# Kernel tuning notes

Hardware: AMD Instinct MI355X
Metric: run time of the kernel (lower is better)

## Reference

```python
import jax, jax.numpy as jnp
import numpy as np

N = 50000      # nodes
E = 800000     # edges (avg degree 16)
F_IN = 128     # num_node_features
D = 64         # embedding_size (= per-head out_channels)
H = 4          # heads
ED = 20        # edge_dim (hardcoded in module)
SLOPE = 0.2    # GATv2 leaky_relu negative slope
N_LAYERS = 3   # conv applied 3 times with shared weights


def setup_inputs() -> dict:
    key = jax.random.key(0)
    ks = jax.random.split(key, 12)
    s = 0.1
    return {
        "x": jax.random.normal(ks[0], (N, F_IN), jnp.float32),
        "edge_attr": jax.random.normal(ks[1], (E, 2), jnp.float32),
        "edge_index": jax.random.randint(ks[2], (2, E), 0, N, dtype=jnp.int32),
        # f: Linear(F_IN, D)
        "f_W": jax.random.normal(ks[3], (F_IN, D), jnp.float32) * s,
        "f_b": jnp.zeros((D,), jnp.float32),
        # fe: Linear(2, ED)
        "fe_W": jax.random.normal(ks[4], (2, ED), jnp.float32) * s,
        "fe_b": jnp.zeros((ED,), jnp.float32),
        # GATv2Conv lin_l / lin_r: Linear(D, H*D)
        "Wl": jax.random.normal(ks[5], (D, H * D), jnp.float32) * s,
        "bl": jnp.zeros((H * D,), jnp.float32),
        "Wr": jax.random.normal(ks[6], (D, H * D), jnp.float32) * s,
        "br": jnp.zeros((H * D,), jnp.float32),
        # lin_edge: Linear(ED, H*D, bias=False)
        "We": jax.random.normal(ks[7], (ED, H * D), jnp.float32) * s,
        # attention vector att: [H, D]
        "att": jax.random.normal(ks[8], (H, D), jnp.float32) * s,
        # final bias (concat=False -> size D)
        "bias": jnp.zeros((D,), jnp.float32),
    }


def _gatv2_conv(h, e_emb, src, dst, Wl, bl, Wr, br, We, att, bias):
    # h: [N, D], e_emb: [E, ED], src/dst: [E]
    xl = (h @ Wl + bl).reshape(-1, H, D)        # source transform  [N,H,D]
    xr = (h @ Wr + br).reshape(-1, H, D)        # target transform  [N,H,D]
    ee = (e_emb @ We).reshape(-1, H, D)         # edge transform    [E,H,D]
    m = jax.nn.leaky_relu(xl[src] + xr[dst] + ee, SLOPE)  # [E,H,D]
    score = jnp.einsum('ehd,hd->eh', m, att)    # [E,H]
    # segment softmax over incoming edges of each dst node
    smax = jax.ops.segment_max(score, dst, num_segments=N)   # [N,H]
    ex = jnp.exp(score - smax[dst])
    denom = jax.ops.segment_sum(ex, dst, num_segments=N)     # [N,H]
    alpha = ex / denom[dst]                                  # [E,H]
    out = jax.ops.segment_sum(alpha[:, :, None] * xl[src], dst, num_segments=N)  # [N,H,D]
    return out.mean(axis=1) + bias              # concat=False -> head mean, [N,D]


def reference(x, edge_attr, edge_index, f_W, f_b, fe_W, fe_b, Wl, bl, Wr, br, We, att, bias):
    src, dst = edge_index[0], edge_index[1]
    h = jax.nn.relu(x @ f_W + f_b)
    e = jax.nn.relu(edge_attr @ fe_W + fe_b)
    for _ in range(N_LAYERS):
        h = jax.nn.relu(_gatv2_conv(h, e, src, dst, Wl, bl, Wr, br, We, att, bias))
    return h
```

## Files before the change

### kernel.cpp

```cpp
#include <hip/hip_runtime.h>
#include <math.h>

typedef float v2f __attribute__((ext_vector_type(2)));

#define LN2_INV 1.4426950408889634f

__device__ __forceinline__ float fexp2(float x) {
#if __has_builtin(__builtin_amdgcn_exp2f)
    return __builtin_amdgcn_exp2f(x);
#else
    return exp2f(x);
#endif
}

__device__ __forceinline__ int rdlane_i(int v, int k) {
    return __builtin_amdgcn_readlane(v, k);
}

__device__ __forceinline__ v2f max2(v2f a, float b) {
    v2f r; r.x = fmaxf(a.x, b); r.y = fmaxf(a.y, b); return r;
}
__device__ __forceinline__ v2f min2(v2f a, float b) {
    v2f r; r.x = fminf(a.x, b); r.y = fminf(a.y, b); return r;
}

#define DPP_ROW_ADD(V, CTRL) \
    V += __int_as_float(__builtin_amdgcn_update_dpp(0, __float_as_int(V), CTRL, 0xf, 0xf, true));

__global__ __launch_bounds__(256) void k_h0(const float* __restrict__ x,
                                            const float* __restrict__ fW,
                                            const float* __restrict__ fb,
                                            float* __restrict__ h0) {
    __shared__ __align__(16) float xs[8 * 128];
    int t = threadIdx.x;
    int base = blockIdx.x * 8;
#pragma unroll
    for (int r = 0; r < 4; ++r) { int j = r * 256 + t; xs[j] = x[base * 128 + j]; }
    __syncthreads();
    int c = t & 63, half = t >> 6;
    float acc0 = fb[c], acc1 = fb[c];
    int m0 = half, m1 = half + 4;
#pragma unroll 8
    for (int k0 = 0; k0 < 128; k0 += 4) {
        float4 a = *(const float4*)&xs[m0 * 128 + k0];
        float4 b = *(const float4*)&xs[m1 * 128 + k0];
        float w0 = fW[(k0 + 0) * 64 + c], w1 = fW[(k0 + 1) * 64 + c];
        float w2 = fW[(k0 + 2) * 64 + c], w3 = fW[(k0 + 3) * 64 + c];
        acc0 = fmaf(a.x, w0, fmaf(a.y, w1, fmaf(a.z, w2, fmaf(a.w, w3, acc0))));
        acc1 = fmaf(b.x, w0, fmaf(b.y, w1, fmaf(b.z, w2, fmaf(b.w, w3, acc1))));
    }
    h0[(base + m0) * 64 + c] = fmaxf(acc0, 0.f);
    h0[(base + m1) * 64 + c] = fmaxf(acc1, 0.f);
}

__global__ __launch_bounds__(256) void k_xlxr(const float* __restrict__ h,
                                              const float* __restrict__ Wl,
                                              const float* __restrict__ Wr,
                                              const float* __restrict__ bl,
                                              const float* __restrict__ br,
                                              float* __restrict__ xl,
                                              float* __restrict__ xr) {
    __shared__ __align__(16) float hs[16 * 64];
    int t = threadIdx.x;
    int base = blockIdx.x * 16;
#pragma unroll
    for (int r = 0; r < 4; ++r) hs[r * 256 + t] = h[base * 64 + r * 256 + t];
    __syncthreads();
    float bL = bl[t], bR = br[t];
    float accl[16], accr[16];
#pragma unroll
    for (int m = 0; m < 16; ++m) { accl[m] = bL; accr[m] = bR; }
#pragma unroll 4
    for (int k0 = 0; k0 < 64; k0 += 4) {
        float wl[4], wr[4];
#pragma unroll
        for (int q = 0; q < 4; ++q) {
            wl[q] = Wl[(k0 + q) * 256 + t];
            wr[q] = Wr[(k0 + q) * 256 + t];
        }
#pragma unroll
        for (int m = 0; m < 16; ++m) {
            float4 hv = *(const float4*)&hs[m * 64 + k0];
            accl[m] = fmaf(hv.x, wl[0], fmaf(hv.y, wl[1], fmaf(hv.z, wl[2], fmaf(hv.w, wl[3], accl[m]))));
            accr[m] = fmaf(hv.x, wr[0], fmaf(hv.y, wr[1], fmaf(hv.z, wr[2], fmaf(hv.w, wr[3], accr[m]))));
        }
    }
#pragma unroll
    for (int m = 0; m < 16; ++m) {
        xl[(base + m) * 256 + t] = accl[m];
        xr[(base + m) * 256 + t] = accr[m];
    }
}

__global__ void k_zero(int* __restrict__ deg, int* __restrict__ counter, int Nn) {
    int i = blockIdx.x * 256 + threadIdx.x;
    if (i < Nn) deg[i] = 0;
    if (i == 0) *counter = 0;
}

__global__ void k_count(const int* __restrict__ dstArr, int* __restrict__ deg, int Ee) {
    int e = blockIdx.x * 256 + threadIdx.x;
    if (e < Ee) atomicAdd(&deg[dstArr[e]], 1);
}

__global__ void k_alloc(const int* __restrict__ deg, int* __restrict__ counter,
                        int* __restrict__ start, int* __restrict__ cursor, int Nn) {
    int n = blockIdx.x * 256 + threadIdx.x;
    if (n < Nn) {
        int d = deg[n];
        int b = atomicAdd(counter, d);
        start[n] = b;
        cursor[n] = b;
    }
}

__global__ void k_fill(const int* __restrict__ dstArr, const int* __restrict__ srcArr,
                       const float* __restrict__ eattr, const float* __restrict__ feW,
                       const float* __restrict__ feb, int* __restrict__ cursor,
                       int* __restrict__ rec, int Ee) {
    int e = blockIdx.x * 256 + threadIdx.x;
    if (e >= Ee) return;
    float a0 = eattr[2 * e], a1 = eattr[2 * e + 1];
    int p = atomicAdd(&cursor[dstArr[e]], 1);
    float* r = (float*)(rec + (size_t)p * 24);
    float s[20];
#pragma unroll
    for (int k = 0; k < 20; ++k)
        s[k] = fmaxf(fmaf(a0, feW[k], fmaf(a1, feW[20 + k], feb[k])), 0.f);
#pragma unroll
    for (int j = 0; j < 5; ++j)
        ((float4*)r)[j] = make_float4(s[4 * j], s[4 * j + 1], s[4 * j + 2], s[4 * j + 3]);
    ((int*)r)[20] = srcArr[e];
}

__global__ __launch_bounds__(256, 3) void k_edge(
    const float4* __restrict__ xl4p, const float4* __restrict__ xr4p,
    const float* __restrict__ att, const float4* __restrict__ We4,
    const int* __restrict__ rec, const int* __restrict__ start,
    const int* __restrict__ deg, const float* __restrict__ bias,
    float* __restrict__ hout, int Nn) {
    const int lane = threadIdx.x & 63;
    const int n = (int)((blockIdx.x * 256u + threadIdx.x) >> 6);
    if (n >= Nn) return;

    const int dn = __builtin_amdgcn_readfirstlane(deg[n]);
    float4 bias4 = ((const float4*)bias)[lane & 15];
    if (dn == 0) {
        if (lane < 16) {
            float4 o = make_float4(fmaxf(bias4.x, 0.f), fmaxf(bias4.y, 0.f),
                                   fmaxf(bias4.z, 0.f), fmaxf(bias4.w, 0.f));
            ((float4*)hout)[(size_t)n * 16 + lane] = o;
        }
        return;
    }
    const int s0 = __builtin_amdgcn_readfirstlane(start[n]);
    const int* rb = rec + (size_t)s0 * 24 + (lane & 31);

    float4 attv = ((const float4*)att)[lane];
    v2f att01 = {attv.x * LN2_INV, attv.y * LN2_INV};
    v2f att23 = {attv.z * LN2_INV, attv.w * LN2_INV};
    v2f at201 = 0.2f * att01, at223 = 0.2f * att23;
    float4 xrv = xr4p[(size_t)n * 64 + lane];
    v2f xr01 = {xrv.x, xrv.y}, xr23 = {xrv.z, xrv.w};
    v2f we01[20], we23[20];
#pragma unroll
    for (int k = 0; k < 20; ++k) {
        float4 w = We4[k * 64 + lane];
        we01[k].x = w.x; we01[k].y = w.y;
        we23[k].x = w.z; we23[k].y = w.w;
    }
    const int bperm = ((lane & 48) | 15) << 2;

    v2f acc01 = {0.f, 0.f}, acc23 = {0.f, 0.f};
    float l = 0.f;

    int i1 = dn > 1 ? 1 : 0;
    int rv0 = rb[0];
    int rv1 = rb[(size_t)i1 * 24];
    int src0 = rdlane_i(rv0, 20);
    float4 xl0 = xl4p[(size_t)src0 * 64 + lane];

    for (int i = 0; i < dn; ++i) {
        int i2 = (i + 2 < dn) ? (i + 2) : (dn - 1);
        int rv2 = rb[(size_t)i2 * 24];
        int src1 = rdlane_i(rv1, 20);
        float4 xl1 = xl4p[(size_t)src1 * 64 + lane];

        v2f xl01 = {xl0.x, xl0.y}, xl23 = {xl0.z, xl0.w};

        v2f ee01, ee23;
        {
            float sk = __int_as_float(rdlane_i(rv0, 0));
            ee01 = sk * we01[0];
            ee23 = sk * we23[0];
        }
#pragma unroll
        for (int k = 1; k < 20; ++k) {
            float sk = __int_as_float(rdlane_i(rv0, k));
            ee01 += sk * we01[k];
            ee23 += sk * we23[k];
        }

        v2f v01 = (xl01 + xr01) + ee01;
        v2f v23 = (xl23 + xr23) + ee23;
        v2f p01 = att01 * max2(v01, 0.f) + at201 * min2(v01, 0.f);
        v2f p23 = att23 * max2(v23, 0.f) + at223 * min2(v23, 0.f);
        v2f pr = p01 + p23;
        float ps = pr.x + pr.y;
        DPP_ROW_ADD(ps, 0x111)
        DPP_ROW_ADD(ps, 0x112)
        DPP_ROW_ADD(ps, 0x114)
        DPP_ROW_ADD(ps, 0x118)
        float sc = __int_as_float(
            __builtin_amdgcn_ds_bpermute(bperm, __float_as_int(ps)));
        float w_ = fexp2(sc);
        l += w_;
        acc01 += w_ * xl01;
        acc23 += w_ * xl23;

        rv0 = rv1; rv1 = rv2; xl0 = xl1;
    }

    float inv = 0.25f / l;
    float4 r = make_float4(acc01.x * inv, acc01.y * inv, acc23.x * inv, acc23.y * inv);
    r.x += __shfl_xor(r.x, 16, 64); r.x += __shfl_xor(r.x, 32, 64);
    r.y += __shfl_xor(r.y, 16, 64); r.y += __shfl_xor(r.y, 32, 64);
    r.z += __shfl_xor(r.z, 16, 64); r.z += __shfl_xor(r.z, 32, 64);
    r.w += __shfl_xor(r.w, 16, 64); r.w += __shfl_xor(r.w, 32, 64);
    if (lane < 16) {
        float4 o = make_float4(fmaxf(r.x + bias4.x, 0.f), fmaxf(r.y + bias4.y, 0.f),
                               fmaxf(r.z + bias4.z, 0.f), fmaxf(r.w + bias4.w, 0.f));
        ((float4*)hout)[(size_t)n * 16 + lane] = o;
    }
}

extern "C" void kernel_launch(void* const* d_in, const int* in_sizes, int n_in,
                              void* d_out, int out_size, void* d_ws, size_t ws_size,
                              hipStream_t stream) {
    const float* x     = (const float*)d_in[0];
    const float* eattr = (const float*)d_in[1];
    const int*   eidx  = (const int*)d_in[2];
    const float* fW    = (const float*)d_in[3];
    const float* fb    = (const float*)d_in[4];
    const float* feW   = (const float*)d_in[5];
    const float* feb   = (const float*)d_in[6];
    const float* Wl    = (const float*)d_in[7];
    const float* bl    = (const float*)d_in[8];
    const float* Wr    = (const float*)d_in[9];
    const float* br    = (const float*)d_in[10];
    const float* We    = (const float*)d_in[11];
    const float* att   = (const float*)d_in[12];
    const float* bias  = (const float*)d_in[13];
    float* out = (float*)d_out;

    const int N = in_sizes[0] / 128;
    const int E = in_sizes[1] / 2;
    const int* srcArr = eidx;
    const int* dstArr = eidx + E;

    char* p = (char*)d_ws;
    auto alloc = [&](size_t bytes) -> char* {
        char* r = p;
        p += (bytes + 255) & ~(size_t)255;
        return r;
    };
    float* hA   = (float*)alloc((size_t)N * 64 * 4);
    float* hB   = (float*)alloc((size_t)N * 64 * 4);
    float* xl   = (float*)alloc((size_t)N * 256 * 4);
    float* xr   = (float*)alloc((size_t)N * 256 * 4);
    int* deg    = (int*)alloc((size_t)N * 4);
    int* start  = (int*)alloc((size_t)N * 4);
    int* cursor = (int*)alloc((size_t)N * 4);
    int* counter = (int*)alloc(256);
    int* rec    = (int*)alloc((size_t)E * 24 * 4);

    k_h0<<<N / 8, 256, 0, stream>>>(x, fW, fb, hA);
    k_zero<<<(N + 255) / 256, 256, 0, stream>>>(deg, counter, N);
    k_count<<<(E + 255) / 256, 256, 0, stream>>>(dstArr, deg, E);
    k_alloc<<<(N + 255) / 256, 256, 0, stream>>>(deg, counter, start, cursor, N);
    k_fill<<<(E + 255) / 256, 256, 0, stream>>>(dstArr, srcArr, eattr, feW, feb,
                                                cursor, rec, E);

    const float* hin = hA;
    for (int layer = 0; layer < 3; ++layer) {
        float* hout = (layer == 2) ? out : ((layer == 0) ? hB : hA);
        k_xlxr<<<N / 16, 256, 0, stream>>>(hin, Wl, Wr, bl, br, xl, xr);
        k_edge<<<(N * 64) / 256, 256, 0, stream>>>(
            (const float4*)xl, (const float4*)xr, att, (const float4*)We,
            rec, start, deg, bias, hout, N);
        hin = hout;
    }
}
```

Before: 919.2 us.

## Process edges in groups of four with LDS-staged edge weights

The edge kernel now stages the edge-transform weights We in LDS per block instead of holding them in 40 registers per lane. It handles incoming edges four at a time, software-pipelining the record loads and source-row gathers of the next group behind the current group's math. Partial tail groups are masked by zeroing their softmax weight. Leaky-relu is rewritten as a*v + b*|v| with attention and log2 scaling folded in. The aim is to amortise weight reads across four edges, expose more memory-level parallelism and cut register pressure, at the cost of extra LDS reads, redundant work on masked tail edges, and a block-wide barrier before the early return.

```diff
diff --git a/kernel.cpp b/kernel.cpp
--- a/kernel.cpp
+++ b/kernel.cpp
@@ -15,13 +15,6 @@
 
 __device__ __forceinline__ int rdlane_i(int v, int k) {
     return __builtin_amdgcn_readlane(v, k);
-}
-
-__device__ __forceinline__ v2f max2(v2f a, float b) {
-    v2f r; r.x = fmaxf(a.x, b); r.y = fmaxf(a.y, b); return r;
-}
-__device__ __forceinline__ v2f min2(v2f a, float b) {
-    v2f r; r.x = fminf(a.x, b); r.y = fminf(a.y, b); return r;
 }
 
 #define DPP_ROW_ADD(V, CTRL) \
@@ -139,8 +132,14 @@
     const int* __restrict__ rec, const int* __restrict__ start,
     const int* __restrict__ deg, const float* __restrict__ bias,
     float* __restrict__ hout, int Nn) {
-    const int lane = threadIdx.x & 63;
-    const int n = (int)((blockIdx.x * 256u + threadIdx.x) >> 6);
+    __shared__ __align__(16) float4 swe[20 * 64];
+    const int t = threadIdx.x;
+#pragma unroll
+    for (int j = 0; j < 5; ++j) swe[j * 256 + t] = We4[j * 256 + t];
+    __syncthreads();
+
+    const int lane = t & 63;
+    const int n = (int)((blockIdx.x * 256u + t) >> 6);
     if (n >= Nn) return;
 
     const int dn = __builtin_amdgcn_readfirstlane(deg[n]);
@@ -157,69 +156,126 @@
     const int* rb = rec + (size_t)s0 * 24 + (lane & 31);
 
     float4 attv = ((const float4*)att)[lane];
-    v2f att01 = {attv.x * LN2_INV, attv.y * LN2_INV};
-    v2f att23 = {attv.z * LN2_INV, attv.w * LN2_INV};
-    v2f at201 = 0.2f * att01, at223 = 0.2f * att23;
+    float4 aA = make_float4(0.6f * LN2_INV * attv.x, 0.6f * LN2_INV * attv.y,
+                            0.6f * LN2_INV * attv.z, 0.6f * LN2_INV * attv.w);
+    float4 aB = make_float4(0.4f * LN2_INV * attv.x, 0.4f * LN2_INV * attv.y,
+                            0.4f * LN2_INV * attv.z, 0.4f * LN2_INV * attv.w);
     float4 xrv = xr4p[(size_t)n * 64 + lane];
     v2f xr01 = {xrv.x, xrv.y}, xr23 = {xrv.z, xrv.w};
-    v2f we01[20], we23[20];
-#pragma unroll
-    for (int k = 0; k < 20; ++k) {
-        float4 w = We4[k * 64 + lane];
-        we01[k].x = w.x; we01[k].y = w.y;
-        we23[k].x = w.z; we23[k].y = w.w;
-    }
     const int bperm = ((lane & 48) | 15) << 2;
 
     v2f acc01 = {0.f, 0.f}, acc23 = {0.f, 0.f};
     float l = 0.f;
 
-    int i1 = dn > 1 ? 1 : 0;
-    int rv0 = rb[0];
-    int rv1 = rb[(size_t)i1 * 24];
-    int src0 = rdlane_i(rv0, 20);
-    float4 xl0 = xl4p[(size_t)src0 * 64 + lane];
-
-    for (int i = 0; i < dn; ++i) {
-        int i2 = (i + 2 < dn) ? (i + 2) : (dn - 1);
-        int rv2 = rb[(size_t)i2 * 24];
-        int src1 = rdlane_i(rv1, 20);
-        float4 xl1 = xl4p[(size_t)src1 * 64 + lane];
-
-        v2f xl01 = {xl0.x, xl0.y}, xl23 = {xl0.z, xl0.w};
-
-        v2f ee01, ee23;
+    const int nfull = dn >> 2;
+    const int rem = dn & 3;
+    const int ngroups = nfull + (rem ? 1 : 0);
+    const int fb = dn >= 4 ? dn - 4 : 0;
+
+#define LOAD_GROUP(RV, B)                                                   \
+    {                                                                       \
+        _Pragma("unroll")                                                   \
+        for (int j_ = 0; j_ < 4; ++j_) {                                    \
+            int idx_ = (B) + j_;                                            \
+            idx_ = idx_ < dn ? idx_ : dn - 1;                               \
+            RV[j_] = rb[(size_t)idx_ * 24];                                 \
+        }                                                                   \
+    }
+#define GATHER_GROUP(XL, RV)                                                \
+    {                                                                       \
+        _Pragma("unroll")                                                   \
+        for (int j_ = 0; j_ < 4; ++j_) {                                    \
+            int src_ = rdlane_i(RV[j_], 20);                                \
+            XL[j_] = xl4p[(size_t)src_ * 64 + lane];                        \
+        }                                                                   \
+    }
+
+    int rvA[4], rvB[4];
+    float4 xlA[4], xlB[4];
+    int b0 = (nfull > 0) ? 0 : fb;
+    LOAD_GROUP(rvA, b0)
+    GATHER_GROUP(xlA, rvA)
+
+    for (int g = 0; g < ngroups; ++g) {
+        int gn = g + 1;
+        bool havenext = gn < ngroups;
+        if (havenext) {
+            int bn = (gn < nfull) ? (gn << 2) : fb;
+            LOAD_GROUP(rvB, bn)
+        }
+
+        v2f ee01[4], ee23[4];
         {
-            float sk = __int_as_float(rdlane_i(rv0, 0));
-            ee01 = sk * we01[0];
-            ee23 = sk * we23[0];
+            float4 w = swe[lane];
+            v2f w01 = {w.x, w.y}, w23 = {w.z, w.w};
+#pragma unroll
+            for (int j = 0; j < 4; ++j) {
+                float sk = __int_as_float(rdlane_i(rvA[j], 0));
+                ee01[j] = sk * w01;
+                ee23[j] = sk * w23;
+            }
         }
 #pragma unroll
         for (int k = 1; k < 20; ++k) {
-            float sk = __int_as_float(rdlane_i(rv0, k));
-            ee01 += sk * we01[k];
-            ee23 += sk * we23[k];
-        }
-
-        v2f v01 = (xl01 + xr01) + ee01;
-        v2f v23 = (xl23 + xr23) + ee23;
-        v2f p01 = att01 * max2(v01, 0.f) + at201 * min2(v01, 0.f);
-        v2f p23 = att23 * max2(v23, 0.f) + at223 * min2(v23, 0.f);
-        v2f pr = p01 + p23;
-        float ps = pr.x + pr.y;
-        DPP_ROW_ADD(ps, 0x111)
-        DPP_ROW_ADD(ps, 0x112)
-        DPP_ROW_ADD(ps, 0x114)
-        DPP_ROW_ADD(ps, 0x118)
-        float sc = __int_as_float(
-            __builtin_amdgcn_ds_bpermute(bperm, __float_as_int(ps)));
-        float w_ = fexp2(sc);
-        l += w_;
-        acc01 += w_ * xl01;
-        acc23 += w_ * xl23;
-
-        rv0 = rv1; rv1 = rv2; xl0 = xl1;
-    }
+            float4 w = swe[k * 64 + lane];
+            v2f w01 = {w.x, w.y}, w23 = {w.z, w.w};
+#pragma unroll
+            for (int j = 0; j < 4; ++j) {
+                float sk = __int_as_float(rdlane_i(rvA[j], k));
+                ee01[j] += sk * w01;
+                ee23[j] += sk * w23;
+            }
+        }
+
+        if (havenext) GATHER_GROUP(xlB, rvB)
+
+        int b = (g < nfull) ? (g << 2) : fb;
+        int lo = (g < nfull) ? b : (nfull << 2);
+        float ps[4];
+#pragma unroll
+        for (int j = 0; j < 4; ++j) {
+            v2f v01 = {xlA[j].x, xlA[j].y};
+            v2f v23 = {xlA[j].z, xlA[j].w};
+            v01 = (v01 + xr01) + ee01[j];
+            v23 = (v23 + xr23) + ee23[j];
+            float tt = aB.x * __builtin_fabsf(v01.x);
+            tt = fmaf(aA.x, v01.x, tt);
+            tt = fmaf(aB.y, __builtin_fabsf(v01.y), tt);
+            tt = fmaf(aA.y, v01.y, tt);
+            tt = fmaf(aB.z, __builtin_fabsf(v23.x), tt);
+            tt = fmaf(aA.z, v23.x, tt);
+            tt = fmaf(aB.w, __builtin_fabsf(v23.y), tt);
+            tt = fmaf(aA.w, v23.y, tt);
+            ps[j] = tt;
+        }
+#pragma unroll
+        for (int j = 0; j < 4; ++j) { DPP_ROW_ADD(ps[j], 0x111) }
+#pragma unroll
+        for (int j = 0; j < 4; ++j) { DPP_ROW_ADD(ps[j], 0x112) }
+#pragma unroll
+        for (int j = 0; j < 4; ++j) { DPP_ROW_ADD(ps[j], 0x114) }
+#pragma unroll
+        for (int j = 0; j < 4; ++j) { DPP_ROW_ADD(ps[j], 0x118) }
+#pragma unroll
+        for (int j = 0; j < 4; ++j) {
+            float sc = __int_as_float(
+                __builtin_amdgcn_ds_bpermute(bperm, __float_as_int(ps[j])));
+            float mk = (b + j >= lo && b + j < dn) ? 1.f : 0.f;
+            float w_ = fexp2(sc) * mk;
+            l += w_;
+            v2f xl01 = {xlA[j].x, xlA[j].y};
+            v2f xl23 = {xlA[j].z, xlA[j].w};
+            acc01 += w_ * xl01;
+            acc23 += w_ * xl23;
+        }
+
+        if (havenext) {
+#pragma unroll
+            for (int j = 0; j < 4; ++j) { rvA[j] = rvB[j]; xlA[j] = xlB[j]; }
+        }
+    }
+#undef LOAD_GROUP
+#undef GATHER_GROUP
 
     float inv = 0.25f / l;
     float4 r = make_float4(acc01.x * inv, acc01.y * inv, acc23.x * inv, acc23.y * inv);
@@ -272,7 +328,7 @@
     int* start  = (int*)alloc((size_t)N * 4);
     int* cursor = (int*)alloc((size_t)N * 4);
     int* counter = (int*)alloc(256);
-    int* rec    = (int*)alloc((size_t)E * 24 * 4);
+    int* rec    = (int*)alloc((size_t)E * 24 * 4 + 256);
 
     k_h0<<<N / 8, 256, 0, stream>>>(x, fW, fb, hA);
     k_zero<<<(N + 255) / 256, 256, 0, stream>>>(deg, counter, N);
```

Result: slower. 1.089 ms (+18.5%).

## Stage edge weights in LDS, process edges in pairs, simplify leaky-relu scoring

Applied to the files above, without the earlier changes.

Moves the 20x256 edge-transform weight matrix out of per-thread registers into shared memory loaded once per block, which frees registers so occupancy can rise to 4 blocks per SIMD. Edge records are now read as uniform scalar loads instead of per-lane loads plus readlane, and edges are processed two at a time with a two-edge prefetch of source features. The leaky-relu plus attention dot is rewritten as 0.6*att*v + 0.4*att*|v|, which saves min/max operations. In exchange every block pays an LDS fill and barrier, and each inner iteration adds LDS reads for the weights.

```diff
diff --git a/kernel.cpp b/kernel.cpp
--- a/kernel.cpp
+++ b/kernel.cpp
@@ -11,17 +11,6 @@
 #else
     return exp2f(x);
 #endif
-}
-
-__device__ __forceinline__ int rdlane_i(int v, int k) {
-    return __builtin_amdgcn_readlane(v, k);
-}
-
-__device__ __forceinline__ v2f max2(v2f a, float b) {
-    v2f r; r.x = fmaxf(a.x, b); r.y = fmaxf(a.y, b); return r;
-}
-__device__ __forceinline__ v2f min2(v2f a, float b) {
-    v2f r; r.x = fminf(a.x, b); r.y = fminf(a.y, b); return r;
 }
 
 #define DPP_ROW_ADD(V, CTRL) \
@@ -133,14 +122,20 @@
     ((int*)r)[20] = srcArr[e];
 }
 
-__global__ __launch_bounds__(256, 3) void k_edge(
+__global__ __launch_bounds__(256, 4) void k_edge(
     const float4* __restrict__ xl4p, const float4* __restrict__ xr4p,
     const float* __restrict__ att, const float4* __restrict__ We4,
     const int* __restrict__ rec, const int* __restrict__ start,
     const int* __restrict__ deg, const float* __restrict__ bias,
     float* __restrict__ hout, int Nn) {
-    const int lane = threadIdx.x & 63;
-    const int n = (int)((blockIdx.x * 256u + threadIdx.x) >> 6);
+    __shared__ __align__(16) float4 swe[20 * 64];
+    const int t = threadIdx.x;
+#pragma unroll
+    for (int j = 0; j < 5; ++j) swe[j * 256 + t] = We4[j * 256 + t];
+    __syncthreads();
+
+    const int lane = t & 63;
+    const int n = (int)((blockIdx.x * 256u + t) >> 6);
     if (n >= Nn) return;
 
     const int dn = __builtin_amdgcn_readfirstlane(deg[n]);
@@ -154,71 +149,109 @@
         return;
     }
     const int s0 = __builtin_amdgcn_readfirstlane(start[n]);
-    const int* rb = rec + (size_t)s0 * 24 + (lane & 31);
+    const float* __restrict__ rbf = (const float*)rec + (size_t)s0 * 24;
 
     float4 attv = ((const float4*)att)[lane];
-    v2f att01 = {attv.x * LN2_INV, attv.y * LN2_INV};
-    v2f att23 = {attv.z * LN2_INV, attv.w * LN2_INV};
-    v2f at201 = 0.2f * att01, at223 = 0.2f * att23;
+    float4 aA = make_float4(0.6f * LN2_INV * attv.x, 0.6f * LN2_INV * attv.y,
+                            0.6f * LN2_INV * attv.z, 0.6f * LN2_INV * attv.w);
+    float4 aB = make_float4(0.4f * LN2_INV * attv.x, 0.4f * LN2_INV * attv.y,
+                            0.4f * LN2_INV * attv.z, 0.4f * LN2_INV * attv.w);
     float4 xrv = xr4p[(size_t)n * 64 + lane];
     v2f xr01 = {xrv.x, xrv.y}, xr23 = {xrv.z, xrv.w};
-    v2f we01[20], we23[20];
-#pragma unroll
-    for (int k = 0; k < 20; ++k) {
-        float4 w = We4[k * 64 + lane];
-        we01[k].x = w.x; we01[k].y = w.y;
-        we23[k].x = w.z; we23[k].y = w.w;
-    }
     const int bperm = ((lane & 48) | 15) << 2;
 
     v2f acc01 = {0.f, 0.f}, acc23 = {0.f, 0.f};
     float l = 0.f;
 
-    int i1 = dn > 1 ? 1 : 0;
-    int rv0 = rb[0];
-    int rv1 = rb[(size_t)i1 * 24];
-    int src0 = rdlane_i(rv0, 20);
+    const int ngroups = (dn + 1) >> 1;
+
+    const float* r0 = rbf;
+    const float* r1 = rbf + (dn > 1 ? 24 : 0);
+    int src0 = ((const int*)r0)[20];
+    int src1 = ((const int*)r1)[20];
     float4 xl0 = xl4p[(size_t)src0 * 64 + lane];
-
-    for (int i = 0; i < dn; ++i) {
-        int i2 = (i + 2 < dn) ? (i + 2) : (dn - 1);
-        int rv2 = rb[(size_t)i2 * 24];
-        int src1 = rdlane_i(rv1, 20);
-        float4 xl1 = xl4p[(size_t)src1 * 64 + lane];
-
-        v2f xl01 = {xl0.x, xl0.y}, xl23 = {xl0.z, xl0.w};
-
-        v2f ee01, ee23;
+    float4 xl1 = xl4p[(size_t)src1 * 64 + lane];
+
+    for (int g = 0; g < ngroups; ++g) {
+        const bool havenext = (g + 1) < ngroups;
+        const float *nr0, *nr1;
+        float4 nxl0, nxl1;
+        if (havenext) {
+            int e0n = (g + 1) << 1;
+            int e1n = e0n + 1 < dn ? e0n + 1 : dn - 1;
+            nr0 = rbf + (size_t)e0n * 24;
+            nr1 = rbf + (size_t)e1n * 24;
+            int ns0 = ((const int*)nr0)[20];
+            int ns1 = ((const int*)nr1)[20];
+            nxl0 = xl4p[(size_t)ns0 * 64 + lane];
+            nxl1 = xl4p[(size_t)ns1 * 64 + lane];
+        }
+
+        v2f eA01, eA23, eB01, eB23;
         {
-            float sk = __int_as_float(rdlane_i(rv0, 0));
-            ee01 = sk * we01[0];
-            ee23 = sk * we23[0];
+            float4 w = swe[lane];
+            v2f w01 = {w.x, w.y}, w23 = {w.z, w.w};
+            float sa = r0[0], sb = r1[0];
+            eA01 = sa * w01; eA23 = sa * w23;
+            eB01 = sb * w01; eB23 = sb * w23;
         }
 #pragma unroll
         for (int k = 1; k < 20; ++k) {
-            float sk = __int_as_float(rdlane_i(rv0, k));
-            ee01 += sk * we01[k];
-            ee23 += sk * we23[k];
-        }
-
-        v2f v01 = (xl01 + xr01) + ee01;
-        v2f v23 = (xl23 + xr23) + ee23;
-        v2f p01 = att01 * max2(v01, 0.f) + at201 * min2(v01, 0.f);
-        v2f p23 = att23 * max2(v23, 0.f) + at223 * min2(v23, 0.f);
-        v2f pr = p01 + p23;
-        float ps = pr.x + pr.y;
-        DPP_ROW_ADD(ps, 0x111)
-        DPP_ROW_ADD(ps, 0x112)
-        DPP_ROW_ADD(ps, 0x114)
-        DPP_ROW_ADD(ps, 0x118)
-        float sc = __int_as_float(
-            __builtin_amdgcn_ds_bpermute(bperm, __float_as_int(ps)));
-        float w_ = fexp2(sc);
-        l += w_;
-        acc01 += w_ * xl01;
-        acc23 += w_ * xl23;
-
-        rv0 = rv1; rv1 = rv2; xl0 = xl1;
+            float4 w = swe[k * 64 + lane];
+            v2f w01 = {w.x, w.y}, w23 = {w.z, w.w};
+            float sa = r0[k], sb = r1[k];
+            eA01 += sa * w01; eA23 += sa * w23;
+            eB01 += sb * w01; eB23 += sb * w23;
+        }
+
+        {
+            v2f v01 = ((v2f){xl0.x, xl0.y} + xr01) + eA01;
+            v2f v23 = ((v2f){xl0.z, xl0.w} + xr23) + eA23;
+            float tt = aB.x * __builtin_fabsf(v01.x);
+            tt = fmaf(aA.x, v01.x, tt);
+            tt = fmaf(aB.y, __builtin_fabsf(v01.y), tt);
+            tt = fmaf(aA.y, v01.y, tt);
+            tt = fmaf(aB.z, __builtin_fabsf(v23.x), tt);
+            tt = fmaf(aA.z, v23.x, tt);
+            tt = fmaf(aB.w, __builtin_fabsf(v23.y), tt);
+            tt = fmaf(aA.w, v23.y, tt);
+            DPP_ROW_ADD(tt, 0x111)
+            DPP_ROW_ADD(tt, 0x112)
+            DPP_ROW_ADD(tt, 0x114)
+            DPP_ROW_ADD(tt, 0x118)
+            float sc = __int_as_float(
+                __builtin_amdgcn_ds_bpermute(bperm, __float_as_int(tt)));
+            float w_ = fexp2(sc);
+            l += w_;
+            acc01 += w_ * (v2f){xl0.x, xl0.y};
+            acc23 += w_ * (v2f){xl0.z, xl0.w};
+        }
+        if ((g << 1) + 1 < dn) {
+            v2f v01 = ((v2f){xl1.x, xl1.y} + xr01) + eB01;
+            v2f v23 = ((v2f){xl1.z, xl1.w} + xr23) + eB23;
+            float tt = aB.x * __builtin_fabsf(v01.x);
+            tt = fmaf(aA.x, v01.x, tt);
+            tt = fmaf(aB.y, __builtin_fabsf(v01.y), tt);
+            tt = fmaf(aA.y, v01.y, tt);
+            tt = fmaf(aB.z, __builtin_fabsf(v23.x), tt);
+            tt = fmaf(aA.z, v23.x, tt);
+            tt = fmaf(aB.w, __builtin_fabsf(v23.y), tt);
+            tt = fmaf(aA.w, v23.y, tt);
+            DPP_ROW_ADD(tt, 0x111)
+            DPP_ROW_ADD(tt, 0x112)
+            DPP_ROW_ADD(tt, 0x114)
+            DPP_ROW_ADD(tt, 0x118)
+            float sc = __int_as_float(
+                __builtin_amdgcn_ds_bpermute(bperm, __float_as_int(tt)));
+            float w_ = fexp2(sc);
+            l += w_;
+            acc01 += w_ * (v2f){xl1.x, xl1.y};
+            acc23 += w_ * (v2f){xl1.z, xl1.w};
+        }
+
+        if (havenext) {
+            r0 = nr0; r1 = nr1; xl0 = nxl0; xl1 = nxl1;
+        }
     }
 
     float inv = 0.25f / l;
@@ -272,7 +305,7 @@
     int* start  = (int*)alloc((size_t)N * 4);
     int* cursor = (int*)alloc((size_t)N * 4);
     int* counter = (int*)alloc(256);
-    int* rec    = (int*)alloc((size_t)E * 24 * 4);
+    int* rec    = (int*)alloc((size_t)E * 24 * 4 + 256);
 
     k_h0<<<N / 8, 256, 0, stream>>>(x, fW, fb, hA);
     k_zero<<<(N + 255) / 256, 256, 0, stream>>>(deg, counter, N);
```

Result: slower. 985.3 us (+7.2%).

## Sort nodes by degree, stream packed edge weights, use packed FMA in edge kernel

Applied to the files above, without the earlier changes.

Adds a counting sort that orders destination nodes by descending degree so waves with similar work are scheduled together and long nodes start first. The per-lane register-resident We copy (40 v2f) is replaced by a repacked We buffer read from cache each edge, which frees registers and raises the occupancy hint from 3 to 4 waves. The edge transform uses inline v_pk_fma_f32 over pairs of edge features, and leaky-relu is rewritten with an abs-based formula. The cost is extra memory loads of We for every edge plus several small setup kernels.

```diff
diff --git a/kernel.cpp b/kernel.cpp
--- a/kernel.cpp
+++ b/kernel.cpp
@@ -17,12 +17,8 @@
     return __builtin_amdgcn_readlane(v, k);
 }
 
-__device__ __forceinline__ v2f max2(v2f a, float b) {
-    v2f r; r.x = fmaxf(a.x, b); r.y = fmaxf(a.y, b); return r;
-}
-__device__ __forceinline__ v2f min2(v2f a, float b) {
-    v2f r; r.x = fminf(a.x, b); r.y = fminf(a.y, b); return r;
-}
+#define PKFMA(ACC, A, B) \
+    asm("v_pk_fma_f32 %0, %1, %2, %0" : "+v"(ACC) : "v"(A), "v"(B));
 
 #define DPP_ROW_ADD(V, CTRL) \
     V += __int_as_float(__builtin_amdgcn_update_dpp(0, __float_as_int(V), CTRL, 0xf, 0xf, true));
@@ -92,6 +88,14 @@
     }
 }
 
+__global__ void k_wepk(const float* __restrict__ We, float* __restrict__ Wepk) {
+    int t = blockIdx.x * 256 + threadIdx.x;
+    if (t < 10 * 64 * 8) {
+        int p = t & 1, d = (t >> 1) & 3, L = (t >> 3) & 63, kp = t >> 9;
+        Wepk[t] = We[(2 * kp + p) * 256 + 4 * L + d];
+    }
+}
+
 __global__ void k_zero(int* __restrict__ deg, int* __restrict__ counter, int Nn) {
     int i = blockIdx.x * 256 + threadIdx.x;
     if (i < Nn) deg[i] = 0;
@@ -133,15 +137,50 @@
     ((int*)r)[20] = srcArr[e];
 }
 
-__global__ __launch_bounds__(256, 3) void k_edge(
+__global__ void k_sort0(int* __restrict__ hist, int* __restrict__ hcur) {
+    int t = threadIdx.x;
+    hist[t] = 0;
+    hcur[t] = 0;
+}
+
+__global__ void k_sort1(const int* __restrict__ deg, int* __restrict__ hist, int Nn) {
+    int n = blockIdx.x * 256 + threadIdx.x;
+    if (n < Nn) {
+        int b = 255 - min(deg[n], 255);
+        atomicAdd(&hist[b], 1);
+    }
+}
+
+__global__ void k_sort2(const int* __restrict__ hist, int* __restrict__ hoff) {
+    __shared__ int hs[256];
+    int t = threadIdx.x;
+    hs[t] = hist[t];
+    __syncthreads();
+    int s = 0;
+    for (int j = 0; j < 256; ++j) if (j < t) s += hs[j];
+    hoff[t] = s;
+}
+
+__global__ void k_sort3(const int* __restrict__ deg, const int* __restrict__ hoff,
+                        int* __restrict__ hcur, int* __restrict__ order, int Nn) {
+    int n = blockIdx.x * 256 + threadIdx.x;
+    if (n < Nn) {
+        int b = 255 - min(deg[n], 255);
+        int pos = hoff[b] + atomicAdd(&hcur[b], 1);
+        order[pos] = n;
+    }
+}
+
+__global__ __launch_bounds__(256, 4) void k_edge(
     const float4* __restrict__ xl4p, const float4* __restrict__ xr4p,
-    const float* __restrict__ att, const float4* __restrict__ We4,
+    const float* __restrict__ att, const v2f* __restrict__ wepk,
     const int* __restrict__ rec, const int* __restrict__ start,
-    const int* __restrict__ deg, const float* __restrict__ bias,
-    float* __restrict__ hout, int Nn) {
+    const int* __restrict__ deg, const int* __restrict__ order,
+    const float* __restrict__ bias, float* __restrict__ hout, int Nn) {
     const int lane = threadIdx.x & 63;
-    const int n = (int)((blockIdx.x * 256u + threadIdx.x) >> 6);
-    if (n >= Nn) return;
+    const int wid = (int)((blockIdx.x * 256u + threadIdx.x) >> 6);
+    if (wid >= Nn) return;
+    const int n = order[wid];
 
     const int dn = __builtin_amdgcn_readfirstlane(deg[n]);
     float4 bias4 = ((const float4*)bias)[lane & 15];
@@ -157,21 +196,15 @@
     const int* rb = rec + (size_t)s0 * 24 + (lane & 31);
 
     float4 attv = ((const float4*)att)[lane];
-    v2f att01 = {attv.x * LN2_INV, attv.y * LN2_INV};
-    v2f att23 = {attv.z * LN2_INV, attv.w * LN2_INV};
-    v2f at201 = 0.2f * att01, at223 = 0.2f * att23;
+    float4 aA = make_float4(0.6f * LN2_INV * attv.x, 0.6f * LN2_INV * attv.y,
+                            0.6f * LN2_INV * attv.z, 0.6f * LN2_INV * attv.w);
+    float4 aB = make_float4(0.4f * LN2_INV * attv.x, 0.4f * LN2_INV * attv.y,
+                            0.4f * LN2_INV * attv.z, 0.4f * LN2_INV * attv.w);
     float4 xrv = xr4p[(size_t)n * 64 + lane];
-    v2f xr01 = {xrv.x, xrv.y}, xr23 = {xrv.z, xrv.w};
-    v2f we01[20], we23[20];
-#pragma unroll
-    for (int k = 0; k < 20; ++k) {
-        float4 w = We4[k * 64 + lane];
-        we01[k].x = w.x; we01[k].y = w.y;
-        we23[k].x = w.z; we23[k].y = w.w;
-    }
     const int bperm = ((lane & 48) | 15) << 2;
-
-    v2f acc01 = {0.f, 0.f}, acc23 = {0.f, 0.f};
+    const v2f* wp = wepk + (size_t)lane * 4;
+
+    float acc0 = 0.f, acc1 = 0.f, acc2 = 0.f, acc3 = 0.f;
     float l = 0.f;
 
     int i1 = dn > 1 ? 1 : 0;
@@ -186,43 +219,53 @@
         int src1 = rdlane_i(rv1, 20);
         float4 xl1 = xl4p[(size_t)src1 * 64 + lane];
 
-        v2f xl01 = {xl0.x, xl0.y}, xl23 = {xl0.z, xl0.w};
-
-        v2f ee01, ee23;
-        {
-            float sk = __int_as_float(rdlane_i(rv0, 0));
-            ee01 = sk * we01[0];
-            ee23 = sk * we23[0];
+        v2f a0v = {0.f, 0.f}, a1v = {0.f, 0.f}, a2v = {0.f, 0.f}, a3v = {0.f, 0.f};
+#pragma unroll
+        for (int kp = 0; kp < 10; ++kp) {
+            v2f skp;
+            skp.x = __int_as_float(rdlane_i(rv0, 2 * kp));
+            skp.y = __int_as_float(rdlane_i(rv0, 2 * kp + 1));
+            v2f w0 = wp[kp * 256 + 0];
+            v2f w1 = wp[kp * 256 + 1];
+            v2f w2 = wp[kp * 256 + 2];
+            v2f w3 = wp[kp * 256 + 3];
+            PKFMA(a0v, skp, w0)
+            PKFMA(a1v, skp, w1)
+            PKFMA(a2v, skp, w2)
+            PKFMA(a3v, skp, w3)
         }
-#pragma unroll
-        for (int k = 1; k < 20; ++k) {
-            float sk = __int_as_float(rdlane_i(rv0, k));
-            ee01 += sk * we01[k];
-            ee23 += sk * we23[k];
-        }
-
-        v2f v01 = (xl01 + xr01) + ee01;
-        v2f v23 = (xl23 + xr23) + ee23;
-        v2f p01 = att01 * max2(v01, 0.f) + at201 * min2(v01, 0.f);
-        v2f p23 = att23 * max2(v23, 0.f) + at223 * min2(v23, 0.f);
-        v2f pr = p01 + p23;
-        float ps = pr.x + pr.y;
-        DPP_ROW_ADD(ps, 0x111)
-        DPP_ROW_ADD(ps, 0x112)
-        DPP_ROW_ADD(ps, 0x114)
-        DPP_ROW_ADD(ps, 0x118)
+
+        float v0 = (xl0.x + xrv.x) + (a0v.x + a0v.y);
+        float v1 = (xl0.y + xrv.y) + (a1v.x + a1v.y);
+        float v2 = (xl0.z + xrv.z) + (a2v.x + a2v.y);
+        float v3 = (xl0.w + xrv.w) + (a3v.x + a3v.y);
+
+        float tt = aB.x * __builtin_fabsf(v0);
+        tt = fmaf(aA.x, v0, tt);
+        tt = fmaf(aB.y, __builtin_fabsf(v1), tt);
+        tt = fmaf(aA.y, v1, tt);
+        tt = fmaf(aB.z, __builtin_fabsf(v2), tt);
+        tt = fmaf(aA.z, v2, tt);
+        tt = fmaf(aB.w, __builtin_fabsf(v3), tt);
+        tt = fmaf(aA.w, v3, tt);
+        DPP_ROW_ADD(tt, 0x111)
+        DPP_ROW_ADD(tt, 0x112)
+        DPP_ROW_ADD(tt, 0x114)
+        DPP_ROW_ADD(tt, 0x118)
         float sc = __int_as_float(
-            __builtin_amdgcn_ds_bpermute(bperm, __float_as_int(ps)));
+            __builtin_amdgcn_ds_bpermute(bperm, __float_as_int(tt)));
         float w_ = fexp2(sc);
         l += w_;
-        acc01 += w_ * xl01;
-        acc23 += w_ * xl23;
+        acc0 = fmaf(w_, xl0.x, acc0);
+        acc1 = fmaf(w_, xl0.y, acc1);
+        acc2 = fmaf(w_, xl0.z, acc2);
+        acc3 = fmaf(w_, xl0.w, acc3);
 
         rv0 = rv1; rv1 = rv2; xl0 = xl1;
     }
 
     float inv = 0.25f / l;
-    float4 r = make_float4(acc01.x * inv, acc01.y * inv, acc23.x * inv, acc23.y * inv);
+    float4 r = make_float4(acc0 * inv, acc1 * inv, acc2 * inv, acc3 * inv);
     r.x += __shfl_xor(r.x, 16, 64); r.x += __shfl_xor(r.x, 32, 64);
     r.y += __shfl_xor(r.y, 16, 64); r.y += __shfl_xor(r.y, 32, 64);
     r.z += __shfl_xor(r.z, 16, 64); r.z += __shfl_xor(r.z, 32, 64);
@@ -268,26 +311,36 @@
     float* hB   = (float*)alloc((size_t)N * 64 * 4);
     float* xl   = (float*)alloc((size_t)N * 256 * 4);
     float* xr   = (float*)alloc((size_t)N * 256 * 4);
+    float* Wepk = (float*)alloc(10 * 64 * 8 * 4);
     int* deg    = (int*)alloc((size_t)N * 4);
     int* start  = (int*)alloc((size_t)N * 4);
     int* cursor = (int*)alloc((size_t)N * 4);
     int* counter = (int*)alloc(256);
-    int* rec    = (int*)alloc((size_t)E * 24 * 4);
+    int* hist   = (int*)alloc(256 * 4);
+    int* hoff   = (int*)alloc(256 * 4);
+    int* hcur   = (int*)alloc(256 * 4);
+    int* order  = (int*)alloc((size_t)N * 4);
+    int* rec    = (int*)alloc((size_t)E * 24 * 4 + 256);
 
     k_h0<<<N / 8, 256, 0, stream>>>(x, fW, fb, hA);
+    k_wepk<<<20, 256, 0, stream>>>(We, Wepk);
     k_zero<<<(N + 255) / 256, 256, 0, stream>>>(deg, counter, N);
     k_count<<<(E + 255) / 256, 256, 0, stream>>>(dstArr, deg, E);
     k_alloc<<<(N + 255) / 256, 256, 0, stream>>>(deg, counter, start, cursor, N);
     k_fill<<<(E + 255) / 256, 256, 0, stream>>>(dstArr, srcArr, eattr, feW, feb,
                                                 cursor, rec, E);
+    k_sort0<<<1, 256, 0, stream>>>(hist, hcur);
+    k_sort1<<<(N + 255) / 256, 256, 0, stream>>>(deg, hist, N);
+    k_sort2<<<1, 256, 0, stream>>>(hist, hoff);
+    k_sort3<<<(N + 255) / 256, 256, 0, stream>>>(deg, hoff, hcur, order, N);
 
     const float* hin = hA;
     for (int layer = 0; layer < 3; ++layer) {
         float* hout = (layer == 2) ? out : ((layer == 0) ? hB : hA);
         k_xlxr<<<N / 16, 256, 0, stream>>>(hin, Wl, Wr, bl, br, xl, xr);
         k_edge<<<(N * 64) / 256, 256, 0, stream>>>(
-            (const float4*)xl, (const float4*)xr, att, (const float4*)We,
-            rec, start, deg, bias, hout, N);
+            (const float4*)xl, (const float4*)xr, att, (const v2f*)Wepk,
+            rec, start, deg, order, bias, hout, N);
         hin = hout;
     }
 }
```

Result: slower. 2.101 ms (+128.6%).
